# Kernel tuning notes

Hardware: AMD Instinct MI355X
Metric: run time of the kernel (lower is better)

Reference implementation:

```python
import math
import jax, jax.numpy as jnp
import numpy as np

T, B, E, H = 2048, 1, 2048, 32
HD = E // H          # head_dim = 64
HALF = HD // 2       # rotary half = 32
SCALE_LENGTH = 1024


def duplicate_interleave(m):
    # [S, HALF] -> [S, HD], each column duplicated adjacently
    return jnp.repeat(m, 2, axis=-1)


def rotate_every_two(x):
    # x: [BH, S, HD]
    x1 = x[:, :, ::2]
    x2 = x[:, :, 1::2]
    return jnp.stack((-x2, x1), axis=-1).reshape(x.shape)


def apply_rotary_pos_emb(x, sin, cos, scale):
    # sin/cos/scale: [S, HALF]; x: [BH, S, HD]
    sin2 = duplicate_interleave(sin * scale)
    cos2 = duplicate_interleave(cos * scale)
    return x * cos2 + rotate_every_two(x) * sin2


def setup_inputs() -> dict:
    key = jax.random.key(0)
    ks = jax.random.split(key, 8)
    std = 0.02
    query = jax.random.normal(ks[0], (T, B, E), jnp.float32)
    key_t = jax.random.normal(ks[1], (T, B, E), jnp.float32)
    value = jax.random.normal(ks[2], (T, B, E), jnp.float32)
    Wq = jax.random.normal(ks[3], (E, E), jnp.float32) * std
    Wk = jax.random.normal(ks[4], (E, E), jnp.float32) * std
    Wv = jax.random.normal(ks[5], (E, E), jnp.float32) * std
    Wo = jax.random.normal(ks[6], (E, E), jnp.float32) * std
    bq = jnp.zeros((E,), jnp.float32)
    bk = jnp.zeros((E,), jnp.float32)
    bv = jnp.zeros((E,), jnp.float32)
    bo = jnp.zeros((E,), jnp.float32)
    # XPos-style rotary tables
    pos = jnp.arange(T, dtype=jnp.float32)
    inv_freq = 1.0 / (10000.0 ** (jnp.arange(HALF, dtype=jnp.float32) / HALF))
    ang = pos[:, None] * inv_freq[None, :]          # [T, HALF]
    sin = jnp.sin(ang)
    cos = jnp.cos(ang)
    scale_base = 512.0
    dim_scale = (jnp.arange(0, HD, 2, dtype=jnp.float32) + 0.4 * HD) / (1.4 * HD)
    xscale = dim_scale[None, :] ** (pos[:, None] / scale_base)  # [T, HALF]
    # causal additive mask
    attn_mask = jnp.where(jnp.triu(jnp.ones((T, T), bool), k=1), -1e9, 0.0).astype(jnp.float32)
    return {"query": query, "key": key_t, "value": value,
            "Wq": Wq, "bq": bq, "Wk": Wk, "bk": bk, "Wv": Wv, "bv": bv,
            "Wo": Wo, "bo": bo, "sin": sin, "cos": cos, "xscale": xscale,
            "attn_mask": attn_mask, "scale_length": SCALE_LENGTH}


def reference(query, key, value, Wq, bq, Wk, bk, Wv, bv, Wo, bo,
              sin, cos, xscale, attn_mask, scale_length):
    tgt_len, bsz, embed_dim = query.shape
    scaling = HD ** -0.5

    def proj(x, W, b):
        y = x @ W.T + b                                # [T, B, E]
        return y.reshape(tgt_len, bsz * H, HD).transpose(1, 0, 2)  # [BH, T, HD]

    q = proj(query, Wq, bq)
    k = proj(key, Wk, bk)
    v = proj(value, Wv, bv)

    # self-attention XPos rotary: k scaled by 1/xscale, q by xscale (last q_len rows)
    k = apply_rotary_pos_emb(k, sin, cos, 1.0 / xscale)
    q = apply_rotary_pos_emb(q, sin[-tgt_len:], cos[-tgt_len:], xscale[-tgt_len:])

    src_len = k.shape[1]
    if src_len > scale_length:
        pos_k = jnp.arange(src_len - tgt_len, src_len, dtype=jnp.float32)
        scale_attention = jnp.maximum(1.0, jnp.log(pos_k) / math.log(scale_length))
        q = q * scale_attention[None, :, None]

    q = q * scaling
    attn_weights = jnp.einsum('btd,bsd->bts', q, k)      # [BH, T, S]
    attn_weights = attn_weights + attn_mask[None, :, :]
    attn_weights = jax.nn.softmax(attn_weights.astype(jnp.float32), axis=-1
                                  ).astype(q.dtype)
    attn = jnp.einsum('bts,bsd->btd', attn_weights, v)   # [BH, T, HD]
    attn = attn.transpose(1, 0, 2).reshape(tgt_len, bsz, embed_dim)
    attn = attn @ Wo.T + bo
    return attn
```

## Files before the change

kernel.cpp:

```cpp
#include <hip/hip_runtime.h>
#include <hip/hip_bf16.h>
#include <math.h>

#define T_LEN 2048
#define EMB   2048
#define NH    32
#define HD    64
#define HALF  32

typedef __attribute__((ext_vector_type(8))) short short8v;
typedef __attribute__((ext_vector_type(4))) float floatx4;

__device__ inline void gload_lds16(const void* g, void* l) {
    __builtin_amdgcn_global_load_lds(
        (const __attribute__((address_space(1))) unsigned int*)g,
        (__attribute__((address_space(3))) unsigned int*)l,
        16, 0, 0);
}

__device__ inline ushort f2bf(float x) {
    union { float f; unsigned u; } c; c.f = x;
    const unsigned r = c.u + 0x7FFFu + ((c.u >> 16) & 1u);
    return (ushort)(r >> 16);
}

#define BARRIER() do { asm volatile("" ::: "memory"); \
    __builtin_amdgcn_s_barrier(); asm volatile("" ::: "memory"); } while (0)
#define VMW8() asm volatile("s_waitcnt vmcnt(8)" ::: "memory")
#define VMW4() asm volatile("s_waitcnt vmcnt(4)" ::: "memory")
#define VMW0() asm volatile("s_waitcnt vmcnt(0)" ::: "memory")

__global__ __launch_bounds__(256) void conv_all(
    const float* __restrict__ s0, const float* __restrict__ s1,
    const float* __restrict__ s2, const float* __restrict__ s3,
    const float* __restrict__ s4, const float* __restrict__ s5,
    const float* __restrict__ s6, ushort* __restrict__ dst)
{
    const int idx = blockIdx.x * 256 + threadIdx.x;
    const int t = idx >> 19;
    const int r = (idx & 524287) * 8;
    const float* in = t == 0 ? s0 : t == 1 ? s1 : t == 2 ? s2 : t == 3 ? s3
                    : t == 4 ? s4 : t == 5 ? s5 : s6;
    const float4 v0 = *reinterpret_cast<const float4*>(&in[r]);
    const float4 v1 = *reinterpret_cast<const float4*>(&in[r + 4]);
    ushort o[8];
    o[0] = f2bf(v0.x); o[1] = f2bf(v0.y); o[2] = f2bf(v0.z); o[3] = f2bf(v0.w);
    o[4] = f2bf(v1.x); o[5] = f2bf(v1.y); o[6] = f2bf(v1.z); o[7] = f2bf(v1.w);
    *reinterpret_cast<uint4*>(&dst[(size_t)t * 4194304 + r]) =
        *reinterpret_cast<const uint4*>(o);
}

__global__ __launch_bounds__(256) void rot_tables(
    const float* __restrict__ sinp, const float* __restrict__ cosp,
    const float* __restrict__ xscale,
    float2* __restrict__ qt, float2* __restrict__ kt)
{
    const int idx = blockIdx.x * 256 + threadIdx.x;
    const int t = idx >> 5;
    const float s = sinp[idx], c = cosp[idx], xs = xscale[idx];
    float sa = 1.f;
    if (t >= 2) {
        const float lv = __logf((float)t) * 0.14426950408889634f;
        sa = lv > 1.f ? lv : 1.f;
    }
    const float qs = xs * sa * 0.125f * 1.4426950408889634f;
    qt[idx] = make_float2(c * qs, s * qs);
    const float ks = 1.f / xs;
    kt[idx] = make_float2(c * ks, s * ks);
}

#define QBM 256
#define QBN 256

#define STAGE_A3(tau, h, slot) do {                                            \
    const int _tc = (tau) * 64;                                                \
    _Pragma("unroll") for (int _i = 0; _i < 2; ++_i) {                         \
        gload_lds16(&Ap[(size_t)(bm + (h) * 128 + wid * 16 + _i * 8 + rl) * 2048 + _tc + csw], \
                    &lds[(slot) * 16384 + (h) * 8192 + (wid * 16 + _i * 8) * 64]); \
    } } while (0)

#define STAGE_B2(tau, h, slot) do {                                            \
    const int _tc = (tau) * 64;                                                \
    _Pragma("unroll") for (int _i = 0; _i < 2; ++_i) {                         \
        gload_lds16(&Bp[(size_t)(bn + (h) * 128 + wid * 16 + _i * 8 + rl) * 2048 + _tc + csw], \
                    &lds[49152 + (slot) * 16384 + (h) * 8192 + (wid * 16 + _i * 8) * 64]); \
    } } while (0)

#define PH(sa_, sb_, mp, VMWSTMT, ...) do {                                    \
    if ((mp) == 0) {                                                           \
        _Pragma("unroll") for (int n = 0; n < 4; ++n) {                        \
            bf[n][0] = ldB(sb_, n, 0);                                         \
            bf[n][1] = ldB(sb_, n, 1);                                         \
        }                                                                      \
    }                                                                          \
    af[0][0] = ldA(sa_, (mp) * 2, 0);     af[0][1] = ldA(sa_, (mp) * 2, 1);    \
    af[1][0] = ldA(sa_, (mp) * 2 + 1, 0); af[1][1] = ldA(sa_, (mp) * 2 + 1, 1);\
    __VA_ARGS__;                                                               \
    BARRIER();                                                                 \
    __builtin_amdgcn_s_setprio(1);                                             \
    _Pragma("unroll") for (int mm = 0; mm < 2; ++mm)                           \
    _Pragma("unroll") for (int n = 0; n < 4; ++n)                              \
    _Pragma("unroll") for (int kk = 0; kk < 2; ++kk)                           \
        acc[(mp) * 2 + mm][n] = __builtin_amdgcn_mfma_f32_16x16x32_bf16(       \
            af[mm][kk], bf[n][kk], acc[(mp) * 2 + mm][n], 0, 0, 0);            \
    __builtin_amdgcn_s_setprio(0);                                             \
    VMWSTMT;                                                                   \
    BARRIER();                                                                 \
} while (0)

#define TILE6(sa, sb, sa2, tau2, LASTVMW) do {                                 \
    PH(sa, sb, 0, (void)0, STAGE_A3(tau2, 0, sa2));                            \
    PH(sa, sb, 1, (void)0, STAGE_A3(tau2, 1, sa2));                            \
    PH(sa, sb, 2, (void)0, STAGE_B2(tau2, 0, sb));                             \
    PH(sa, sb, 3, LASTVMW, STAGE_B2(tau2, 1, sb));                             \
} while (0)

__global__ __launch_bounds__(512, 2) void gemm_qkv8(
    const ushort* __restrict__ Astack,
    const ushort* __restrict__ Wstack,
    const float* __restrict__ bq, const float* __restrict__ bk,
    const float* __restrict__ bv,
    ushort* __restrict__ outQ, ushort* __restrict__ outK,
    ushort* __restrict__ outVt,
    const float2* __restrict__ qtab, const float2* __restrict__ ktab)
{
    __shared__ ushort lds[81920];
    const int tid  = threadIdx.x;
    const int lane = tid & 63;
    const int wid  = tid >> 6;

    const int b   = blockIdx.x + blockIdx.y * 24;
    const int xcd = b & 7;
    const int idx = b >> 3;
    const int bx  = xcd * 3 + (idx >> 3);
    const int by  = idx & 7;
    const int which = bx >> 3;
    const int bn  = (bx & 7) * QBN;
    const int bm  = by * QBM;
    const ushort* Ap = Astack + (size_t)which * 4194304;
    const ushort* Bp = Wstack + (size_t)which * 4194304;

    const int rl  = lane >> 3;
    const int csw = (((lane & 7) ^ ((lane >> 3) & 7)) * 8);
    const int lm  = lane & 15;
    const int lg  = lane >> 4;
    const char* ldsb = reinterpret_cast<const char*>(lds);

    auto ldA = [&](int slot, int m, int kk) -> short8v {
        const int row = m * 16 + lm;
        const int off = (slot * 16384 + (wid >> 2) * 8192) * 2 + row * 128
                      + (((kk * 4 + lg) ^ (row & 7)) * 16);
        return *reinterpret_cast<const short8v*>(ldsb + off);
    };
    auto ldB = [&](int slot, int n, int kk) -> short8v {
        const int row = (wid & 1) * 64 + n * 16 + lm;
        const int off = (49152 + slot * 16384 + ((wid & 3) >> 1) * 8192) * 2
                      + row * 128 + (((kk * 4 + lg) ^ (row & 7)) * 16);
        return *reinterpret_cast<const short8v*>(ldsb + off);
    };

    floatx4 acc[8][4] = {};
    short8v bf[4][2];
    short8v af[2][2];

    STAGE_A3(0, 0, 0); STAGE_A3(0, 1, 0);
    STAGE_B2(0, 0, 0); STAGE_B2(0, 1, 0);
    STAGE_A3(1, 0, 1); STAGE_A3(1, 1, 1);
    STAGE_B2(1, 0, 1); STAGE_B2(1, 1, 1);
    VMW8();
    BARRIER();

    for (int i = 0; i < 5; ++i) {
        const int t = 6 * i;
        TILE6(0, 0, 2, t + 2, VMW8());
        TILE6(1, 1, 0, t + 3, VMW8());
        TILE6(2, 0, 1, t + 4, VMW8());
        TILE6(0, 1, 2, t + 5, VMW8());
        TILE6(1, 0, 0, t + 6, VMW8());
        TILE6(2, 1, 1, t + 7, VMW8());
    }
    PH(0, 0, 0, (void)0, (void)0);
    PH(0, 0, 1, (void)0, (void)0);
    PH(0, 0, 2, (void)0, (void)0);
    PH(0, 0, 3, VMW0(),  (void)0);
    PH(1, 1, 0, (void)0, (void)0);
    PH(1, 1, 1, (void)0, (void)0);
    PH(1, 1, 2, (void)0, (void)0);
    PH(1, 1, 3, (void)0, (void)0);

    const float* bias = which == 0 ? bq : which == 1 ? bk : bv;
    const float2* tbl = which == 0 ? qtab : ktab;
    #pragma unroll
    for (int m = 0; m < 8; ++m) {
        #pragma unroll
        for (int n = 0; n < 4; ++n) {
            const int col = bn + (wid & 3) * 64 + n * 16 + lm;
            const float bz = bias[col];
            const int row0 = bm + (wid >> 2) * 128 + m * 16 + lg * 4;
            if (which == 2) {
                ushort o4[4];
                #pragma unroll
                for (int j = 0; j < 4; ++j)
                    o4[j] = f2bf(acc[m][n][j] + bz);
                *reinterpret_cast<uint2*>(&outVt[(size_t)col * T_LEN + row0]) =
                    *reinterpret_cast<const uint2*>(o4);
            } else {
                ushort* O = which == 0 ? outQ : outK;
                const int p = (col & 63) >> 1;
                const bool even = (col & 1) == 0;
                #pragma unroll
                for (int j = 0; j < 4; ++j) {
                    const int row = row0 + j;
                    const float v = acc[m][n][j] + bz;
                    const float pv = __shfl_xor(v, 1);
                    const float2 cs = tbl[row * HALF + p];
                    const float outv = even ? v * cs.x - pv * cs.y
                                            : v * cs.x + pv * cs.y;
                    O[(size_t)row * EMB + col] = f2bf(outv);
                }
            }
        }
    }
}

#define GBM 128
#define GBN 128
#define GBK 64

__global__ __launch_bounds__(256) void gemm_out_sk(
    const ushort* __restrict__ A,
    const ushort* __restrict__ B,
    float* __restrict__ P)
{
    __shared__ ushort As[GBM * GBK];
    __shared__ ushort Bs[GBN * GBK];
    const int tid  = threadIdx.x;
    const int lane = tid & 63;
    const int wid  = tid >> 6;
    const int bm = blockIdx.y * GBM;
    const int bn = blockIdx.x * GBN;
    const int z  = blockIdx.z;
    const int wr = (wid >> 1) * 64;
    const int wc = (wid & 1) * 64;

    floatx4 acc[4][4] = {};

    const int lrow  = lane >> 3;
    const int lcolb = (lane & 7) * 8;

    for (int k0 = z * 1024; k0 < (z + 1) * 1024; k0 += GBK) {
        #pragma unroll
        for (int c = 0; c < 4; ++c) {
            const int chunk = wid * 4 + c;
            const int row = chunk * 8 + lrow;
            gload_lds16(&A[(size_t)(bm + row) * EMB + k0 + lcolb], &As[chunk * 512]);
            gload_lds16(&B[(size_t)(bn + row) * EMB + k0 + lcolb], &Bs[chunk * 512]);
        }
        __syncthreads();
        #pragma unroll
        for (int kk = 0; kk < 2; ++kk) {
            short8v a[4], b[4];
            #pragma unroll
            for (int m = 0; m < 4; ++m)
                a[m] = *reinterpret_cast<const short8v*>(
                    &As[(wr + m * 16 + (lane & 15)) * GBK + kk * 32 + (lane >> 4) * 8]);
            #pragma unroll
            for (int n = 0; n < 4; ++n)
                b[n] = *reinterpret_cast<const short8v*>(
                    &Bs[(wc + n * 16 + (lane & 15)) * GBK + kk * 32 + (lane >> 4) * 8]);
            #pragma unroll
            for (int m = 0; m < 4; ++m)
                #pragma unroll
                for (int n = 0; n < 4; ++n)
                    acc[m][n] = __builtin_amdgcn_mfma_f32_16x16x32_bf16(
                        a[m], b[n], acc[m][n], 0, 0, 0);
        }
        __syncthreads();
    }

    float* Pz = P + (size_t)z * 4194304;
    const int cr = (lane >> 4) * 4;
    const int cc = lane & 15;
    #pragma unroll
    for (int m = 0; m < 4; ++m) {
        #pragma unroll
        for (int n = 0; n < 4; ++n) {
            const int col = bn + wc + n * 16 + cc;
            #pragma unroll
            for (int j = 0; j < 4; ++j) {
                const int row = bm + wr + m * 16 + cr + j;
                Pz[(size_t)row * EMB + col] = acc[m][n][j];
            }
        }
    }
}

__global__ __launch_bounds__(256) void reduce_out(
    const float* __restrict__ P, const float* __restrict__ bias,
    float* __restrict__ C)
{
    const int i = (blockIdx.x * 256 + threadIdx.x) * 4;
    const float4 a = *reinterpret_cast<const float4*>(&P[i]);
    const float4 b = *reinterpret_cast<const float4*>(&P[4194304 + i]);
    const float4 bz = *reinterpret_cast<const float4*>(&bias[i & 2047]);
    float4 o;
    o.x = a.x + b.x + bz.x; o.y = a.y + b.y + bz.y;
    o.z = a.z + b.z + bz.z; o.w = a.w + b.w + bz.w;
    *reinterpret_cast<float4*>(&C[i]) = o;
}

__global__ __launch_bounds__(256) void flash_attn_mfma(
    const ushort* __restrict__ Qb,
    const ushort* __restrict__ Kb,
    const ushort* __restrict__ Vt,
    ushort* __restrict__ Ob)
{
    __shared__ ushort Ks[2][64 * 64];
    __shared__ ushort Vs[2][64 * 64];
    __shared__ ushort Ps[4][16 * 64];

    const int h   = blockIdx.x;
    const int qb  = (T_LEN / 64 - 1) - blockIdx.y;
    const int tid = threadIdx.x;
    const int lane = tid & 63;
    const int wid  = tid >> 6;
    const int qrow_w = qb * 64 + wid * 16;
    const int lm = lane & 15;
    const int lg = lane >> 4;

    short8v qf[2];
    {
        const ushort* qp = &Qb[(size_t)(qrow_w + lm) * EMB + h * HD + lg * 8];
        qf[0] = *reinterpret_cast<const short8v*>(qp);
        qf[1] = *reinterpret_cast<const short8v*>(qp + 32);
    }

    floatx4 oacc[4] = {};
    float m = -1e30f, l = 0.f;

    const int srow = lane >> 3;
    const int schk = lane & 7;

    {
        #pragma unroll
        for (int i = 0; i < 2; ++i) {
            const int slot = wid * 2 + i;
            const int row  = slot * 8 + srow;
            const int cswz = (schk ^ (row & 7)) * 8;
            gload_lds16(&Kb[(size_t)row * EMB + h * HD + cswz], &Ks[0][slot * 512]);
            gload_lds16(&Vt[(size_t)(h * HD + row) * T_LEN + cswz], &Vs[0][slot * 512]);
        }
    }
    __syncthreads();

    for (int kb = 0; kb <= qb; ++kb) {
        const int cur = kb & 1;
        if (kb < qb) {
            const int nkb = kb + 1;
            #pragma unroll
            for (int i = 0; i < 2; ++i) {
                const int slot = wid * 2 + i;
                const int row  = slot * 8 + srow;
                const int cswz = (schk ^ (row & 7)) * 8;
                gload_lds16(&Kb[(size_t)(nkb * 64 + row) * EMB + h * HD + cswz],
                            &Ks[cur ^ 1][slot * 512]);
                gload_lds16(&Vt[(size_t)(h * HD + row) * T_LEN + nkb * 64 + cswz],
                            &Vs[cur ^ 1][slot * 512]);
            }
        }

        float sv[16];
        #pragma unroll
        for (int t = 0; t < 4; ++t) {
            floatx4 sacc = {};
            const int srow_l = t * 16 + lm;
            const char* krow = reinterpret_cast<const char*>(Ks[cur]) + srow_l * 128;
            const int swz = (srow_l & 7) << 4;
            #pragma unroll
            for (int kk = 0; kk < 2; ++kk) {
                const int cb = (kk * 64 + lg * 16) ^ swz;
                short8v kf = *reinterpret_cast<const short8v*>(krow + cb);
                sacc = __builtin_amdgcn_mfma_f32_16x16x32_bf16(kf, qf[kk], sacc, 0, 0, 0);
            }
            sv[t * 4 + 0] = sacc[0]; sv[t * 4 + 1] = sacc[1];
            sv[t * 4 + 2] = sacc[2]; sv[t * 4 + 3] = sacc[3];
        }

        const int qg = qrow_w + lm;
        if (kb == qb) {
            #pragma unroll
            for (int t = 0; t < 4; ++t)
                #pragma unroll
                for (int r = 0; r < 4; ++r) {
                    const int sg = kb * 64 + t * 16 + lg * 4 + r;
                    if (sg > qg) sv[t * 4 + r] = -1e30f;
                }
        }

        float mx = sv[0];
        #pragma unroll
        for (int i = 1; i < 16; ++i) mx = fmaxf(mx, sv[i]);
        mx = fmaxf(mx, __shfl_xor(mx, 16));
        mx = fmaxf(mx, __shfl_xor(mx, 32));
        float corr = 1.f;
        if (!__all(mx - m <= 11.544f)) {
            const float mnew = fmaxf(m, mx);
            corr = exp2f(m - mnew);
            m = mnew;
            float corr4[4];
            #pragma unroll
            for (int r = 0; r < 4; ++r)
                corr4[r] = __shfl(corr, lg * 4 + r);
            #pragma unroll
            for (int td = 0; td < 4; ++td)
                #pragma unroll
                for (int r = 0; r < 4; ++r)
                    oacc[td][r] *= corr4[r];
        }
        float ps = 0.f;
        unsigned pw[8];
        #pragma unroll
        for (int i = 0; i < 8; ++i) {
            const float p0 = exp2f(sv[2 * i + 0] - m);
            const float p1 = exp2f(sv[2 * i + 1] - m);
            ps += p0 + p1;
            const __hip_bfloat162 h2 = __float22bfloat162_rn(make_float2(p0, p1));
            pw[i] = *reinterpret_cast<const unsigned*>(&h2);
        }
        ps += __shfl_xor(ps, 16);
        ps += __shfl_xor(ps, 32);
        l = l * corr + ps;

        {
            char* pbase = reinterpret_cast<char*>(&Ps[wid][0]) + lm * 128;
            const int swz = (lm & 7) << 4;
            #pragma unroll
            for (int t = 0; t < 4; ++t) {
                uint2 w;
                w.x = pw[2 * t + 0];
                w.y = pw[2 * t + 1];
                const int cb = (t * 32 + lg * 8) ^ swz;
                *reinterpret_cast<uint2*>(pbase + cb) = w;
            }
        }

        const char* pwave = reinterpret_cast<const char*>(&Ps[wid][0]);
        #pragma unroll
        for (int kk = 0; kk < 2; ++kk) {
            const int acb = (kk * 64 + lg * 16) ^ ((lm & 7) << 4);
            short8v pa = *reinterpret_cast<const short8v*>(pwave + lm * 128 + acb);
            #pragma unroll
            for (int td = 0; td < 4; ++td) {
                const int d = td * 16 + lm;
                const int bcb = (kk * 64 + lg * 16) ^ ((d & 7) << 4);
                short8v vb = *reinterpret_cast<const short8v*>(
                    reinterpret_cast<const char*>(Vs[cur]) + d * 128 + bcb);
                oacc[td] = __builtin_amdgcn_mfma_f32_16x16x32_bf16(pa, vb, oacc[td], 0, 0, 0);
            }
        }

        __syncthreads();
    }

    float invl[4];
    #pragma unroll
    for (int r = 0; r < 4; ++r)
        invl[r] = 1.f / __shfl(l, lg * 4 + r);
    #pragma unroll
    for (int td = 0; td < 4; ++td) {
        #pragma unroll
        for (int r = 0; r < 4; ++r) {
            const int trow = qrow_w + lg * 4 + r;
            const int col  = h * HD + td * 16 + lm;
            Ob[(size_t)trow * EMB + col] = f2bf(oacc[td][r] * invl[r]);
        }
    }
}

extern "C" void kernel_launch(void* const* d_in, const int* in_sizes, int n_in,
                              void* d_out, int out_size, void* d_ws, size_t ws_size,
                              hipStream_t stream) {
    const float* query = (const float*)d_in[0];
    const float* key   = (const float*)d_in[1];
    const float* value = (const float*)d_in[2];
    const float* Wq = (const float*)d_in[3];
    const float* bq = (const float*)d_in[4];
    const float* Wk = (const float*)d_in[5];
    const float* bk = (const float*)d_in[6];
    const float* Wv = (const float*)d_in[7];
    const float* bv = (const float*)d_in[8];
    const float* Wo = (const float*)d_in[9];
    const float* bo = (const float*)d_in[10];
    const float* sinp   = (const float*)d_in[11];
    const float* cosp   = (const float*)d_in[12];
    const float* xscale = (const float*)d_in[13];
    float* out = (float*)d_out;

    const size_t MB = 1024 * 1024;
    char* ws = (char*)d_ws;
    ushort* bWqkv = (ushort*)(ws + 0 * MB);
    ushort* bWo   = (ushort*)(ws + 24 * MB);
    ushort* bAqkv = (ushort*)(ws + 32 * MB);
    ushort* bQ  = (ushort*)(ws + 56 * MB);
    ushort* bK  = (ushort*)(ws + 64 * MB);
    ushort* bVt = (ushort*)(ws + 72 * MB);
    ushort* bAo = (ushort*)(ws + 80 * MB);
    float2* qtab = (float2*)(ws + 88 * MB);
    float2* ktab = (float2*)(ws + 88 * MB + 512 * 1024);
    float*  Pout = (float*)(ws + 32 * MB);

    conv_all<<<7 * 524288 / 256, 256, 0, stream>>>(
        Wq, Wk, Wv, Wo, query, key, value, bWqkv);
    rot_tables<<<T_LEN * HALF / 256, 256, 0, stream>>>(
        sinp, cosp, xscale, qtab, ktab);

    dim3 gQKV(24, 8);
    gemm_qkv8<<<gQKV, 512, 0, stream>>>(bAqkv, bWqkv, bq, bk, bv,
                                        bQ, bK, bVt, qtab, ktab);

    dim3 gFlash(NH, T_LEN / 64);
    flash_attn_mfma<<<gFlash, 256, 0, stream>>>(bQ, bK, bVt, bAo);

    dim3 gOut(EMB / GBN, T_LEN / GBM, 2);
    gemm_out_sk<<<gOut, 256, 0, stream>>>(bAo, bWo, Pout);
    reduce_out<<<T_LEN * EMB / (256 * 4), 256, 0, stream>>>(Pout, bo, out);
}
```

Before: 175.7 us.

## Merge rotary table setup into conversion kernel, bf16 split-K partials, flash tweaks

Folds the rotary table computation into the conversion kernel as extra blocks, which removes one kernel launch. The split-K output GEMM now stores its partials as bf16 instead of fp32, halving that intermediate traffic, and the reduce kernel handles 8 elements per thread. In flash attention, s_setprio raises wave priority around the MFMA sections, and the max and sum reductions become trees to shorten dependency chains. Rounding the partials to bf16 adds error to the final fp32 output.

```diff
diff --git a/kernel.cpp b/kernel.cpp
--- a/kernel.cpp
+++ b/kernel.cpp
@@ -27,15 +27,32 @@
 #define BARRIER() do { asm volatile("" ::: "memory"); \
     __builtin_amdgcn_s_barrier(); asm volatile("" ::: "memory"); } while (0)
 #define VMW8() asm volatile("s_waitcnt vmcnt(8)" ::: "memory")
-#define VMW4() asm volatile("s_waitcnt vmcnt(4)" ::: "memory")
 #define VMW0() asm volatile("s_waitcnt vmcnt(0)" ::: "memory")
 
 __global__ __launch_bounds__(256) void conv_all(
     const float* __restrict__ s0, const float* __restrict__ s1,
     const float* __restrict__ s2, const float* __restrict__ s3,
     const float* __restrict__ s4, const float* __restrict__ s5,
-    const float* __restrict__ s6, ushort* __restrict__ dst)
+    const float* __restrict__ s6, ushort* __restrict__ dst,
+    const float* __restrict__ sinp, const float* __restrict__ cosp,
+    const float* __restrict__ xscale,
+    float2* __restrict__ qt, float2* __restrict__ kt)
 {
+    if (blockIdx.x >= 14336) {
+        const int idx = (blockIdx.x - 14336) * 256 + threadIdx.x;
+        const int t = idx >> 5;
+        const float s = sinp[idx], c = cosp[idx], xs = xscale[idx];
+        float sa = 1.f;
+        if (t >= 2) {
+            const float lv = __logf((float)t) * 0.14426950408889634f;
+            sa = lv > 1.f ? lv : 1.f;
+        }
+        const float qs = xs * sa * 0.125f * 1.4426950408889634f;
+        qt[idx] = make_float2(c * qs, s * qs);
+        const float ks = 1.f / xs;
+        kt[idx] = make_float2(c * ks, s * ks);
+        return;
+    }
     const int idx = blockIdx.x * 256 + threadIdx.x;
     const int t = idx >> 19;
     const int r = (idx & 524287) * 8;
@@ -48,25 +65,6 @@
     o[4] = f2bf(v1.x); o[5] = f2bf(v1.y); o[6] = f2bf(v1.z); o[7] = f2bf(v1.w);
     *reinterpret_cast<uint4*>(&dst[(size_t)t * 4194304 + r]) =
         *reinterpret_cast<const uint4*>(o);
-}
-
-__global__ __launch_bounds__(256) void rot_tables(
-    const float* __restrict__ sinp, const float* __restrict__ cosp,
-    const float* __restrict__ xscale,
-    float2* __restrict__ qt, float2* __restrict__ kt)
-{
-    const int idx = blockIdx.x * 256 + threadIdx.x;
-    const int t = idx >> 5;
-    const float s = sinp[idx], c = cosp[idx], xs = xscale[idx];
-    float sa = 1.f;
-    if (t >= 2) {
-        const float lv = __logf((float)t) * 0.14426950408889634f;
-        sa = lv > 1.f ? lv : 1.f;
-    }
-    const float qs = xs * sa * 0.125f * 1.4426950408889634f;
-    qt[idx] = make_float2(c * qs, s * qs);
-    const float ks = 1.f / xs;
-    kt[idx] = make_float2(c * ks, s * ks);
 }
 
 #define QBM 256
@@ -230,7 +228,7 @@
 __global__ __launch_bounds__(256) void gemm_out_sk(
     const ushort* __restrict__ A,
     const ushort* __restrict__ B,
-    float* __restrict__ P)
+    ushort* __restrict__ P)
 {
     __shared__ ushort As[GBM * GBK];
     __shared__ ushort Bs[GBN * GBK];
@@ -278,7 +276,7 @@
         __syncthreads();
     }
 
-    float* Pz = P + (size_t)z * 4194304;
+    ushort* Pz = P + (size_t)z * 4194304;
     const int cr = (lane >> 4) * 4;
     const int cc = lane & 15;
     #pragma unroll
@@ -289,24 +287,32 @@
             #pragma unroll
             for (int j = 0; j < 4; ++j) {
                 const int row = bm + wr + m * 16 + cr + j;
-                Pz[(size_t)row * EMB + col] = acc[m][n][j];
+                Pz[(size_t)row * EMB + col] = f2bf(acc[m][n][j]);
             }
         }
     }
 }
 
 __global__ __launch_bounds__(256) void reduce_out(
-    const float* __restrict__ P, const float* __restrict__ bias,
+    const ushort* __restrict__ P, const float* __restrict__ bias,
     float* __restrict__ C)
 {
-    const int i = (blockIdx.x * 256 + threadIdx.x) * 4;
-    const float4 a = *reinterpret_cast<const float4*>(&P[i]);
-    const float4 b = *reinterpret_cast<const float4*>(&P[4194304 + i]);
-    const float4 bz = *reinterpret_cast<const float4*>(&bias[i & 2047]);
-    float4 o;
-    o.x = a.x + b.x + bz.x; o.y = a.y + b.y + bz.y;
-    o.z = a.z + b.z + bz.z; o.w = a.w + b.w + bz.w;
-    *reinterpret_cast<float4*>(&C[i]) = o;
+    const int i = (blockIdx.x * 256 + threadIdx.x) * 8;
+    const uint4 pa = *reinterpret_cast<const uint4*>(&P[i]);
+    const uint4 pb = *reinterpret_cast<const uint4*>(&P[4194304 + i]);
+    const ushort* ua = reinterpret_cast<const ushort*>(&pa);
+    const ushort* ub = reinterpret_cast<const ushort*>(&pb);
+    const int cb = i & 2047;
+    float o[8];
+    #pragma unroll
+    for (int j = 0; j < 8; ++j) {
+        union { unsigned u; float f; } fa, fb;
+        fa.u = (unsigned)ua[j] << 16;
+        fb.u = (unsigned)ub[j] << 16;
+        o[j] = fa.f + fb.f + bias[cb + j];
+    }
+    *reinterpret_cast<float4*>(&C[i])     = make_float4(o[0], o[1], o[2], o[3]);
+    *reinterpret_cast<float4*>(&C[i + 4]) = make_float4(o[4], o[5], o[6], o[7]);
 }
 
 __global__ __launch_bounds__(256) void flash_attn_mfma(
@@ -370,6 +376,7 @@
         }
 
         float sv[16];
+        __builtin_amdgcn_s_setprio(1);
         #pragma unroll
         for (int t = 0; t < 4; ++t) {
             floatx4 sacc = {};
@@ -385,6 +392,7 @@
             sv[t * 4 + 0] = sacc[0]; sv[t * 4 + 1] = sacc[1];
             sv[t * 4 + 2] = sacc[2]; sv[t * 4 + 3] = sacc[3];
         }
+        __builtin_amdgcn_s_setprio(0);
 
         const int qg = qrow_w + lm;
         if (kb == qb) {
@@ -397,9 +405,11 @@
                 }
         }
 
-        float mx = sv[0];
-        #pragma unroll
-        for (int i = 1; i < 16; ++i) mx = fmaxf(mx, sv[i]);
+        const float mx0 = fmaxf(fmaxf(fmaxf(sv[0], sv[1]), fmaxf(sv[2], sv[3])),
+                                fmaxf(fmaxf(sv[4], sv[5]), fmaxf(sv[6], sv[7])));
+        const float mx1 = fmaxf(fmaxf(fmaxf(sv[8], sv[9]), fmaxf(sv[10], sv[11])),
+                                fmaxf(fmaxf(sv[12], sv[13]), fmaxf(sv[14], sv[15])));
+        float mx = fmaxf(mx0, mx1);
         mx = fmaxf(mx, __shfl_xor(mx, 16));
         mx = fmaxf(mx, __shfl_xor(mx, 32));
         float corr = 1.f;
@@ -417,16 +427,18 @@
                 for (int r = 0; r < 4; ++r)
                     oacc[td][r] *= corr4[r];
         }
-        float ps = 0.f;
+        float psum[8];
         unsigned pw[8];
         #pragma unroll
         for (int i = 0; i < 8; ++i) {
             const float p0 = exp2f(sv[2 * i + 0] - m);
             const float p1 = exp2f(sv[2 * i + 1] - m);
-            ps += p0 + p1;
+            psum[i] = p0 + p1;
             const __hip_bfloat162 h2 = __float22bfloat162_rn(make_float2(p0, p1));
             pw[i] = *reinterpret_cast<const unsigned*>(&h2);
         }
+        float ps = ((psum[0] + psum[1]) + (psum[2] + psum[3]))
+                 + ((psum[4] + psum[5]) + (psum[6] + psum[7]));
         ps += __shfl_xor(ps, 16);
         ps += __shfl_xor(ps, 32);
         l = l * corr + ps;
@@ -445,6 +457,7 @@
         }
 
         const char* pwave = reinterpret_cast<const char*>(&Ps[wid][0]);
+        __builtin_amdgcn_s_setprio(1);
         #pragma unroll
         for (int kk = 0; kk < 2; ++kk) {
             const int acb = (kk * 64 + lg * 16) ^ ((lm & 7) << 4);
@@ -458,6 +471,7 @@
                 oacc[td] = __builtin_amdgcn_mfma_f32_16x16x32_bf16(pa, vb, oacc[td], 0, 0, 0);
             }
         }
+        __builtin_amdgcn_s_setprio(0);
 
         __syncthreads();
     }
@@ -507,11 +521,10 @@
     ushort* bAo = (ushort*)(ws + 80 * MB);
     float2* qtab = (float2*)(ws + 88 * MB);
     float2* ktab = (float2*)(ws + 88 * MB + 512 * 1024);
-    float*  Pout = (float*)(ws + 32 * MB);
-
-    conv_all<<<7 * 524288 / 256, 256, 0, stream>>>(
-        Wq, Wk, Wv, Wo, query, key, value, bWqkv);
-    rot_tables<<<T_LEN * HALF / 256, 256, 0, stream>>>(
+    ushort* Pout = (ushort*)(ws + 32 * MB);
+
+    conv_all<<<14336 + 256, 256, 0, stream>>>(
+        Wq, Wk, Wv, Wo, query, key, value, bWqkv,
         sinp, cosp, xscale, qtab, ktab);
 
     dim3 gQKV(24, 8);
@@ -523,5 +536,5 @@
 
     dim3 gOut(EMB / GBN, T_LEN / GBM, 2);
     gemm_out_sk<<<gOut, 256, 0, stream>>>(bAo, bWo, Pout);
-    reduce_out<<<T_LEN * EMB / (256 * 4), 256, 0, stream>>>(Pout, bo, out);
-}
+    reduce_out<<<T_LEN * EMB / (256 * 8), 256, 0, stream>>>(Pout, bo, out);
+}
```

Result: faster. 171.6 us, median of 2 (-2.3%).
